# Optimization experiments

Hardware: AMD Instinct MI355X
Metric: run time of the kernel (lower is better)

Reference implementation:

```python
import jax, jax.numpy as jnp
import numpy as np

N = 50000    # nodes
P = 4        # meta-paths
E = 800000   # edges per meta-path (avg degree 16)
IN = 256     # in_size
OUT = 128    # out_size


def _xavier(key, shape, gain=1.0):
    fan_in, fan_out = shape[-2], shape[-1]
    lim = gain * np.sqrt(6.0 / (fan_in + fan_out))
    return jax.random.uniform(key, shape, jnp.float32, -lim, lim)


def setup_inputs() -> dict:
    key = jax.random.key(0)
    ks = jax.random.split(key, 8)
    x = jax.random.normal(ks[0], (N, IN), jnp.float32)
    src = jax.random.randint(ks[1], (P, E), 0, N)
    dst = jax.random.randint(ks[2], (P, E), 0, N)
    # per-meta-path GraphConv weight/bias (dgl default: xavier weight, zero bias)
    W = _xavier(ks[3], (P, IN, OUT))
    b_conv = jnp.zeros((P, OUT), jnp.float32)
    # semantic attention vectors, xavier with gain=1.414 on shape (1, OUT)
    att_lim = 1.414 * np.sqrt(6.0 / (1 + OUT))
    att = jax.random.uniform(ks[4], (P, OUT), jnp.float32, -att_lim, att_lim)
    fc_w = _xavier(ks[5], (OUT, OUT))
    fc_b = jnp.zeros((OUT,), jnp.float32)
    h_bias = jnp.zeros((OUT,), jnp.float32)
    return {"x": x, "W": W, "b_conv": b_conv, "att": att,
            "fc_w": fc_w, "fc_b": fc_b, "h_bias": h_bias,
            "src": src, "dst": dst}


def _graphconv(x, src, dst, W, b):
    # dgl GraphConv, norm='both', allow_zero_in_degree=True (degrees clamped to 1)
    ones_e = jnp.ones(src.shape[0], x.dtype)
    deg_out = jnp.maximum(jax.ops.segment_sum(ones_e, src, num_segments=N), 1.0)
    deg_in = jnp.maximum(jax.ops.segment_sum(ones_e, dst, num_segments=N), 1.0)
    # weight applied before aggregation (in_size > out_size path) -- same math
    xw = (x * jax.lax.rsqrt(deg_out)[:, None]) @ W          # [N, OUT]
    agg = jax.ops.segment_sum(xw[src], dst, num_segments=N)  # [N, OUT]
    return agg * jax.lax.rsqrt(deg_in)[:, None] + b


def reference(x, W, b_conv, att, fc_w, fc_b, h_bias, src, dst):
    # one GraphConv per meta-path (P is a small fixed structural set)
    hs = [_graphconv(x, src[i], dst[i], W[i], b_conv[i]) for i in range(P)]
    # semantic attention: sp_i = tanh(fc(h_i)).mean(0); beta_i = att_i . sp_i
    sp = jnp.stack([jnp.tanh(h @ fc_w.T + fc_b).mean(axis=0) for h in hs])  # [P, OUT]
    beta = jax.nn.softmax(jnp.sum(att * sp, axis=-1))  # [P]
    h = hs[0] * beta[0]
    for i in range(1, P):
        h = h + hs[i] * beta[i]
    # epilogue: bias (self_loop=False, activation=None, dropout eval = identity)
    return h + h_bias
```

## Files before the change

### kernel.cpp

```cpp
#include <hip/hip_runtime.h>
#include <math.h>

#define N_NODES 50000
#define P_PATHS 4
#define E_EDGES 800000
#define IN_F 256
#define OUT_F 128
#define NPB 128
#define NBUCK 391
#define NCHUNK 200
#define CHUNK_E (E_EDGES / NCHUNK)
#define GBLK 391
#define DSL 20
#define QTR 4
#define Q_N 12500
#define Q_W 6250
#define AP 264
#define FP 136
#define RSB 196

typedef unsigned short ushort_t;
typedef unsigned int uint_t;
typedef float f32x4 __attribute__((ext_vector_type(4)));
typedef short s16x8 __attribute__((ext_vector_type(8)));

__device__ __forceinline__ ushort_t f2bf(float f) {
    uint_t u = __float_as_uint(f);
    return (ushort_t)((u + 0x7FFFu + ((u >> 16) & 1u)) >> 16);
}
__device__ __forceinline__ float bf2f(ushort_t h) {
    return __uint_as_float(((uint_t)h) << 16);
}

__global__ void prep_kernel(const float* __restrict__ W, const float* __restrict__ fcw,
                            ushort_t* __restrict__ Wt, ushort_t* __restrict__ fcwb)
{
    int idx = blockIdx.x * blockDim.x + threadIdx.x;
    if (idx < P_PATHS * IN_F * OUT_F) {
        int p = idx >> 15;
        int r = idx & 32767;
        int k = r >> 7;
        int n = r & 127;
        Wt[((size_t)p << 15) + (size_t)n * IN_F + k] = f2bf(W[idx]);
    }
    if (idx < OUT_F * OUT_F) fcwb[idx] = f2bf(fcw[idx]);
}

__global__ __launch_bounds__(256) void deghist_kernel(const int* __restrict__ src,
                                                      const int* __restrict__ dst,
                                                      uint_t* __restrict__ dhist,
                                                      uint_t* __restrict__ bcounts)
{
    __shared__ uint_t cnt[Q_W];
    int sl = blockIdx.x, q = blockIdx.y, p = blockIdx.z;
    int t = threadIdx.x;
    if (q == QTR) {
        for (int i = t; i < NBUCK; i += 256) cnt[i] = 0;
        __syncthreads();
        const int4* d4 = (const int4*)(dst + (size_t)p * E_EDGES + (size_t)sl * (E_EDGES / DSL));
        for (int i = t; i < E_EDGES / DSL / 4; i += 256) {
            int4 v = d4[i];
            atomicAdd(&cnt[v.x >> 7], 1u);
            atomicAdd(&cnt[v.y >> 7], 1u);
            atomicAdd(&cnt[v.z >> 7], 1u);
            atomicAdd(&cnt[v.w >> 7], 1u);
        }
        __syncthreads();
        for (int i = t; i < NBUCK; i += 256)
            if (cnt[i]) atomicAdd(&bcounts[p * NBUCK + i], cnt[i]);
        return;
    }
    int nbase = q * Q_N;
    for (int i = t; i < Q_W; i += 256) cnt[i] = 0;
    __syncthreads();
    const int4* s4 = (const int4*)(src + (size_t)p * E_EDGES + (size_t)sl * (E_EDGES / DSL));
    for (int i = t; i < E_EDGES / DSL / 4; i += 256) {
        int4 v = s4[i];
        uint_t r;
        r = (uint_t)(v.x - nbase); if (r < Q_N) atomicAdd(&cnt[r >> 1], 1u << ((r & 1) * 16));
        r = (uint_t)(v.y - nbase); if (r < Q_N) atomicAdd(&cnt[r >> 1], 1u << ((r & 1) * 16));
        r = (uint_t)(v.z - nbase); if (r < Q_N) atomicAdd(&cnt[r >> 1], 1u << ((r & 1) * 16));
        r = (uint_t)(v.w - nbase); if (r < Q_N) atomicAdd(&cnt[r >> 1], 1u << ((r & 1) * 16));
    }
    __syncthreads();
    uint_t* outp = dhist + (((size_t)p * QTR + q) * DSL + sl) * Q_W;
    for (int i = t; i < Q_W; i += 256) outp[i] = cnt[i];
}

__global__ __launch_bounds__(1024) void rsout_bscan_kernel(const uint_t* __restrict__ dhist,
                                                           float* __restrict__ rsout,
                                                           const uint_t* __restrict__ bcounts,
                                                           int* __restrict__ bstart,
                                                           int* __restrict__ bcursor)
{
    int t = threadIdx.x;
    if (blockIdx.x == RSB) {
        __shared__ int a[2048], b[2048];
        for (int i = t; i < 2048; i += 1024)
            a[i] = (i < P_PATHS * NBUCK) ? (int)bcounts[i] : 0;
        __syncthreads();
        int* pin = a; int* pout = b;
        for (int off = 1; off < 2048; off <<= 1) {
            for (int i = t; i < 2048; i += 1024)
                pout[i] = pin[i] + (i >= off ? pin[i - off] : 0);
            __syncthreads();
            int* tmp = pin; pin = pout; pout = tmp;
        }
        for (int i = t; i < P_PATHS * NBUCK; i += 1024) {
            int st = pin[i] - (int)bcounts[i];
            bstart[i] = st;
            bcursor[i] = st;
        }
        if (t == 0) bstart[P_PATHS * NBUCK] = pin[P_PATHS * NBUCK - 1];
        return;
    }
    int idx = blockIdx.x * 1024 + t;
    if (idx >= P_PATHS * QTR * Q_W) return;
    int ph = idx / Q_W;
    int w  = idx % Q_W;
    const uint_t* base = dhist + (size_t)ph * DSL * Q_W + w;
    uint_t s = 0;
#pragma unroll
    for (int sl = 0; sl < DSL; ++sl) s += base[(size_t)sl * Q_W];
    int p = ph >> 2, q = ph & 3;
    int node = q * Q_N + 2 * w;
    uint_t c0 = s & 0xFFFFu, c1 = s >> 16;
    rsout[(size_t)p * N_NODES + node]     = rsqrtf((float)(c0 ? c0 : 1u));
    rsout[(size_t)p * N_NODES + node + 1] = rsqrtf((float)(c1 ? c1 : 1u));
}

__global__ __launch_bounds__(256) void bscatter_kernel(const int* __restrict__ src,
                                                       const int* __restrict__ dst,
                                                       int* __restrict__ bcursor,
                                                       uint_t* __restrict__ ebuf)
{
    __shared__ uint_t bh[NBUCK];
    __shared__ uint_t lbase[NBUCK];
    int p = blockIdx.y;
    int t = threadIdx.x;
    int sub = p * E_EDGES;
    int* bcursor_p = bcursor + p * NBUCK;
    uint_t* ebuf_p = ebuf + (size_t)p * E_EDGES;
    for (int i = t; i < NBUCK; i += 256) bh[i] = 0;
    __syncthreads();
    size_t ebase = (size_t)p * E_EDGES + (size_t)blockIdx.x * CHUNK_E;
    const int4* d4 = (const int4*)(dst + ebase);
    const int4* s4 = (const int4*)(src + ebase);
    for (int i = t; i < CHUNK_E / 4; i += 256) {
        int4 v = d4[i];
        atomicAdd(&bh[v.x >> 7], 1u);
        atomicAdd(&bh[v.y >> 7], 1u);
        atomicAdd(&bh[v.z >> 7], 1u);
        atomicAdd(&bh[v.w >> 7], 1u);
    }
    __syncthreads();
    for (int i = t; i < NBUCK; i += 256) {
        uint_t c = bh[i];
        lbase[i] = c ? (uint_t)(atomicAdd(&bcursor_p[i], (int)c) - sub) : 0u;
        bh[i] = 0;
    }
    __syncthreads();
    for (int i = t; i < CHUNK_E / 4; i += 256) {
        int4 d = d4[i];
        int4 s = s4[i];
        { int bk = d.x >> 7; uint_t pos = lbase[bk] + atomicAdd(&bh[bk], 1u); ebuf_p[pos] = (uint_t)s.x | ((uint_t)(d.x & 127) << 16); }
        { int bk = d.y >> 7; uint_t pos = lbase[bk] + atomicAdd(&bh[bk], 1u); ebuf_p[pos] = (uint_t)s.y | ((uint_t)(d.y & 127) << 16); }
        { int bk = d.z >> 7; uint_t pos = lbase[bk] + atomicAdd(&bh[bk], 1u); ebuf_p[pos] = (uint_t)s.z | ((uint_t)(d.z & 127) << 16); }
        { int bk = d.w >> 7; uint_t pos = lbase[bk] + atomicAdd(&bh[bk], 1u); ebuf_p[pos] = (uint_t)s.w | ((uint_t)(d.w & 127) << 16); }
    }
}

__global__ __launch_bounds__(256) void blocal_kernel(const uint_t* __restrict__ ebuf,
                                                     const int* __restrict__ bstart,
                                                     ushort_t* __restrict__ eidx2,
                                                     int* __restrict__ rsn)
{
    __shared__ uint_t hist[NPB];
    __shared__ uint_t cur[NPB];
    __shared__ uint_t sa[NPB], sb[NPB];
    int bkt = blockIdx.x;
    int p = blockIdx.y;
    int t = threadIdx.x;
    int sub = p * E_EDGES;
    const uint_t* ebuf_p = ebuf + (size_t)p * E_EDGES;
    ushort_t* eidx2_p = eidx2 + (size_t)p * E_EDGES;
    int* rsn_p = rsn + (size_t)p * (N_NODES + 1);
    if (t < NPB) hist[t] = 0;
    __syncthreads();
    int r0 = bstart[p * NBUCK + bkt] - sub;
    int r1 = bstart[p * NBUCK + bkt + 1] - sub;
    for (int e = r0 + t; e < r1; e += 256)
        atomicAdd(&hist[ebuf_p[e] >> 16], 1u);
    __syncthreads();
    if (t < NPB) sa[t] = hist[t];
    __syncthreads();
    uint_t* pin = sa; uint_t* pout = sb;
    for (int off = 1; off < NPB; off <<= 1) {
        if (t < NPB) pout[t] = pin[t] + (t >= off ? pin[t - off] : 0u);
        __syncthreads();
        uint_t* tmp = pin; pin = pout; pout = tmp;
    }
    if (t < NPB) {
        uint_t ex = pin[t] - hist[t];
        int node = bkt * NPB + t;
        if (node < N_NODES) rsn_p[node] = r0 + (int)ex;
        cur[t] = ex;
    }
    if (bkt == NBUCK - 1 && t == 0) rsn_p[N_NODES] = r1;
    __syncthreads();
    for (int e = r0 + t; e < r1; e += 256) {
        uint_t pk = ebuf_p[e];
        int dl = (int)(pk >> 16);
        uint_t pos = atomicAdd(&cur[dl], 1u);
        eidx2_p[r0 + pos] = (ushort_t)(pk & 0xFFFFu);
    }
}

__global__ __launch_bounds__(256) void gemm_xall_kernel(const float* __restrict__ x,
                                                        const ushort_t* __restrict__ Wt,
                                                        const float* __restrict__ rsout,
                                                        ushort_t* __restrict__ xwb)
{
    __shared__ ushort_t As[128 * AP];
    __shared__ ushort_t Bs[128 * AP];
    int m0 = blockIdx.x * 128;
    int t = threadIdx.x;
    int wid = t >> 6, lane = t & 63;
    int wr = wid >> 1, wc = wid & 1;
    int srow = t >> 1, half = (t & 1) * 16;
    int gr = m0 + srow;
#pragma unroll
    for (int c = 0; c < 8; ++c) {
        int kb = c * 32 + half;
        uint4 w0 = make_uint4(0, 0, 0, 0), w1 = make_uint4(0, 0, 0, 0);
        if (gr < N_NODES) {
            const float* ap = x + (size_t)gr * IN_F + kb;
            float4 f0 = *(const float4*)(ap + 0);
            float4 f1 = *(const float4*)(ap + 4);
            float4 f2 = *(const float4*)(ap + 8);
            float4 f3 = *(const float4*)(ap + 12);
            w0.x = (uint_t)f2bf(f0.x) | ((uint_t)f2bf(f0.y) << 16);
            w0.y = (uint_t)f2bf(f0.z) | ((uint_t)f2bf(f0.w) << 16);
            w0.z = (uint_t)f2bf(f1.x) | ((uint_t)f2bf(f1.y) << 16);
            w0.w = (uint_t)f2bf(f1.z) | ((uint_t)f2bf(f1.w) << 16);
            w1.x = (uint_t)f2bf(f2.x) | ((uint_t)f2bf(f2.y) << 16);
            w1.y = (uint_t)f2bf(f2.z) | ((uint_t)f2bf(f2.w) << 16);
            w1.z = (uint_t)f2bf(f3.x) | ((uint_t)f2bf(f3.y) << 16);
            w1.w = (uint_t)f2bf(f3.z) | ((uint_t)f2bf(f3.w) << 16);
        }
        *(uint4*)&As[srow * AP + kb]     = w0;
        *(uint4*)&As[srow * AP + kb + 8] = w1;
    }
    for (int pp = 0; pp < 2; ++pp) {
        int p = blockIdx.y * 2 + pp;
        __syncthreads();
        const ushort_t* Wp = Wt + ((size_t)p << 15);
#pragma unroll
        for (int c = 0; c < 8; ++c) {
            int kb = c * 32 + half;
            const ushort_t* bp = Wp + (size_t)srow * IN_F + kb;
            *(uint4*)&Bs[srow * AP + kb]     = *(const uint4*)(bp);
            *(uint4*)&Bs[srow * AP + kb + 8] = *(const uint4*)(bp + 8);
        }
        __syncthreads();
        f32x4 acc[4][4] = {};
#pragma unroll
        for (int k0 = 0; k0 < IN_F; k0 += 32) {
            s16x8 aF[4], bF[4];
            int kk = k0 + (lane >> 4) * 8;
#pragma unroll
            for (int m = 0; m < 4; ++m)
                aF[m] = *(const s16x8*)&As[(wr * 64 + m * 16 + (lane & 15)) * AP + kk];
#pragma unroll
            for (int n = 0; n < 4; ++n)
                bF[n] = *(const s16x8*)&Bs[(wc * 64 + n * 16 + (lane & 15)) * AP + kk];
#pragma unroll
            for (int m = 0; m < 4; ++m)
#pragma unroll
                for (int n = 0; n < 4; ++n)
                    acc[m][n] = __builtin_amdgcn_mfma_f32_16x16x32_bf16(aF[m], bF[n], acc[m][n], 0, 0, 0);
        }
        ushort_t* xp = xwb + (size_t)p * N_NODES * OUT_F;
        const float* rp = rsout + (size_t)p * N_NODES;
#pragma unroll
        for (int m = 0; m < 4; ++m) {
#pragma unroll
            for (int i = 0; i < 4; ++i) {
                int row = m0 + wr * 64 + m * 16 + (lane >> 4) * 4 + i;
                if (row < N_NODES) {
                    float rs = rp[row];
#pragma unroll
                    for (int n = 0; n < 4; ++n) {
                        int col = wc * 64 + n * 16 + (lane & 15);
                        xp[(size_t)row * OUT_F + col] = f2bf(acc[m][n][i] * rs);
                    }
                }
            }
        }
    }
}

__global__ __launch_bounds__(256) void gather_kernel(const ushort_t* __restrict__ xwb,
                                                     const ushort_t* __restrict__ eidx2,
                                                     const int* __restrict__ rsn,
                                                     const float* __restrict__ bconv,
                                                     uint_t* __restrict__ hb)
{
    int wid = threadIdx.x >> 6, lane = threadIdx.x & 63;
    int p = blockIdx.y;
    int n0 = (blockIdx.x * 4 + wid) * 2;
    const int* rsn_p = rsn + (size_t)p * (N_NODES + 1);
    const ushort_t* eidx2_p = eidx2 + (size_t)p * E_EDGES;
    int bA = rsn_p[n0], mid = rsn_p[n0 + 1], eB = rsn_p[n0 + 2];
    const uint_t* base = (const uint_t*)xwb + (size_t)p * N_NODES * 64 + lane;
    float a0 = 0.f, a1 = 0.f, b0 = 0.f, b1 = 0.f;
    int iA = bA, iB = mid;
    while (iA + 4 <= mid && iB + 4 <= eB) {
        int sA0 = eidx2_p[iA], sA1 = eidx2_p[iA + 1], sA2 = eidx2_p[iA + 2], sA3 = eidx2_p[iA + 3];
        int sB0 = eidx2_p[iB], sB1 = eidx2_p[iB + 1], sB2 = eidx2_p[iB + 2], sB3 = eidx2_p[iB + 3];
        uint_t wA0 = base[(size_t)sA0 * 64];
        uint_t wA1 = base[(size_t)sA1 * 64];
        uint_t wA2 = base[(size_t)sA2 * 64];
        uint_t wA3 = base[(size_t)sA3 * 64];
        uint_t wB0 = base[(size_t)sB0 * 64];
        uint_t wB1 = base[(size_t)sB1 * 64];
        uint_t wB2 = base[(size_t)sB2 * 64];
        uint_t wB3 = base[(size_t)sB3 * 64];
        a0 += (bf2f((ushort_t)wA0) + bf2f((ushort_t)wA1)) + (bf2f((ushort_t)wA2) + bf2f((ushort_t)wA3));
        a1 += (bf2f((ushort_t)(wA0 >> 16)) + bf2f((ushort_t)(wA1 >> 16))) +
              (bf2f((ushort_t)(wA2 >> 16)) + bf2f((ushort_t)(wA3 >> 16)));
        b0 += (bf2f((ushort_t)wB0) + bf2f((ushort_t)wB1)) + (bf2f((ushort_t)wB2) + bf2f((ushort_t)wB3));
        b1 += (bf2f((ushort_t)(wB0 >> 16)) + bf2f((ushort_t)(wB1 >> 16))) +
              (bf2f((ushort_t)(wB2 >> 16)) + bf2f((ushort_t)(wB3 >> 16)));
        iA += 4; iB += 4;
    }
    for (; iA + 4 <= mid; iA += 4) {
        int s0 = eidx2_p[iA], s1 = eidx2_p[iA + 1], s2 = eidx2_p[iA + 2], s3 = eidx2_p[iA + 3];
        uint_t w0 = base[(size_t)s0 * 64];
        uint_t w1 = base[(size_t)s1 * 64];
        uint_t w2 = base[(size_t)s2 * 64];
        uint_t w3 = base[(size_t)s3 * 64];
        a0 += (bf2f((ushort_t)w0) + bf2f((ushort_t)w1)) + (bf2f((ushort_t)w2) + bf2f((ushort_t)w3));
        a1 += (bf2f((ushort_t)(w0 >> 16)) + bf2f((ushort_t)(w1 >> 16))) +
              (bf2f((ushort_t)(w2 >> 16)) + bf2f((ushort_t)(w3 >> 16)));
    }
    for (; iA < mid; ++iA) {
        uint_t w = base[(size_t)eidx2_p[iA] * 64];
        a0 += bf2f((ushort_t)w);
        a1 += bf2f((ushort_t)(w >> 16));
    }
    for (; iB + 4 <= eB; iB += 4) {
        int s0 = eidx2_p[iB], s1 = eidx2_p[iB + 1], s2 = eidx2_p[iB + 2], s3 = eidx2_p[iB + 3];
        uint_t w0 = base[(size_t)s0 * 64];
        uint_t w1 = base[(size_t)s1 * 64];
        uint_t w2 = base[(size_t)s2 * 64];
        uint_t w3 = base[(size_t)s3 * 64];
        b0 += (bf2f((ushort_t)w0) + bf2f((ushort_t)w1)) + (bf2f((ushort_t)w2) + bf2f((ushort_t)w3));
        b1 += (bf2f((ushort_t)(w0 >> 16)) + bf2f((ushort_t)(w1 >> 16))) +
              (bf2f((ushort_t)(w2 >> 16)) + bf2f((ushort_t)(w3 >> 16)));
    }
    for (; iB < eB; ++iB) {
        uint_t w = base[(size_t)eidx2_p[iB] * 64];
        b0 += bf2f((ushort_t)w);
        b1 += bf2f((ushort_t)(w >> 16));
    }
    int dA = mid - bA, dB = eB - mid;
    float scA = rsqrtf((float)(dA > 0 ? dA : 1));
    float scB = rsqrtf((float)(dB > 0 ? dB : 1));
    float2 bc = *(const float2*)(bconv + (size_t)p * OUT_F + 2 * lane);
    hb[((size_t)p * N_NODES + n0) * 64 + lane] =
        (uint_t)f2bf(fmaf(a0, scA, bc.x)) | ((uint_t)f2bf(fmaf(a1, scA, bc.y)) << 16);
    hb[((size_t)p * N_NODES + n0 + 1) * 64 + lane] =
        (uint_t)f2bf(fmaf(b0, scB, bc.x)) | ((uint_t)f2bf(fmaf(b1, scB, bc.y)) << 16);
}

__global__ __launch_bounds__(256) void fc_mfma_kernel(const ushort_t* __restrict__ hb,
                                                      const ushort_t* __restrict__ fcwb,
                                                      const float* __restrict__ fcb,
                                                      float* __restrict__ partial)
{
    __shared__ ushort_t As[128 * FP];
    __shared__ ushort_t Bs[128 * FP];
    __shared__ float red[2][128];
    int m0 = blockIdx.x * 128;
    int p = blockIdx.y;
    int t = threadIdx.x;
    int wid = t >> 6, lane = t & 63;
    int wr = wid >> 1, wc = wid & 1;
    int srow = t >> 1, half = (t & 1) * 16;
    int gr = m0 + srow;
    const ushort_t* hp = hb + (size_t)p * N_NODES * OUT_F;
#pragma unroll
    for (int c = 0; c < 4; ++c) {
        int kb = c * 32 + half;
        uint4 w0 = make_uint4(0, 0, 0, 0), w1 = make_uint4(0, 0, 0, 0);
        if (gr < N_NODES) {
            const ushort_t* ap = hp + (size_t)gr * OUT_F + kb;
            w0 = *(const uint4*)(ap);
            w1 = *(const uint4*)(ap + 8);
        }
        *(uint4*)&As[srow * FP + kb]     = w0;
        *(uint4*)&As[srow * FP + kb + 8] = w1;
        const ushort_t* bp = fcwb + (size_t)srow * OUT_F + kb;
        *(uint4*)&Bs[srow * FP + kb]     = *(const uint4*)(bp);
        *(uint4*)&Bs[srow * FP + kb + 8] = *(const uint4*)(bp + 8);
    }
    __syncthreads();
    f32x4 acc[4][4] = {};
#pragma unroll
    for (int k0 = 0; k0 < OUT_F; k0 += 32) {
        s16x8 aF[4], bF[4];
        int kk = k0 + (lane >> 4) * 8;
#pragma unroll
        for (int m = 0; m < 4; ++m)
            aF[m] = *(const s16x8*)&As[(wr * 64 + m * 16 + (lane & 15)) * FP + kk];
#pragma unroll
        for (int n = 0; n < 4; ++n)
            bF[n] = *(const s16x8*)&Bs[(wc * 64 + n * 16 + (lane & 15)) * FP + kk];
#pragma unroll
        for (int m = 0; m < 4; ++m)
#pragma unroll
            for (int n = 0; n < 4; ++n)
                acc[m][n] = __builtin_amdgcn_mfma_f32_16x16x32_bf16(aF[m], bF[n], acc[m][n], 0, 0, 0);
    }
#pragma unroll
    for (int n = 0; n < 4; ++n) {
        int col = wc * 64 + n * 16 + (lane & 15);
        float fb = fcb[col];
        float s = 0.f;
#pragma unroll
        for (int m = 0; m < 4; ++m)
#pragma unroll
            for (int i = 0; i < 4; ++i) {
                int row = m0 + wr * 64 + m * 16 + (lane >> 4) * 4 + i;
                if (row < N_NODES) s += tanhf(acc[m][n][i] + fb);
            }
        s += __shfl_xor(s, 16);
        s += __shfl_xor(s, 32);
        if (lane < 16) red[wr][col] = s;
    }
    __syncthreads();
    if (t < 128)
        partial[((size_t)p * GBLK + blockIdx.x) * OUT_F + t] = red[0][t] + red[1][t];
}

__global__ __launch_bounds__(512) void beta_reduce_kernel(const float* __restrict__ partial,
                                                          const float* __restrict__ att,
                                                          float* __restrict__ beta)
{
    int t = threadIdx.x;
    int p = t >> 7, c = t & 127;
    float s = 0.f;
    for (int i = 0; i < GBLK; ++i)
        s += partial[((size_t)p * GBLK + i) * OUT_F + c];
    float v = att[p * OUT_F + c] * (s * (1.0f / N_NODES));
    __shared__ float red[512];
    red[t] = v;
    __syncthreads();
    for (int off = 64; off >= 1; off >>= 1) {
        if (c < off) red[t] += red[t + off];
        __syncthreads();
    }
    if (t == 0) {
        float w[P_PATHS], mx = -1e30f;
        for (int q = 0; q < P_PATHS; ++q) { w[q] = red[q * 128]; mx = fmaxf(mx, w[q]); }
        float sum = 0.f;
        for (int q = 0; q < P_PATHS; ++q) { w[q] = expf(w[q] - mx); sum += w[q]; }
        for (int q = 0; q < P_PATHS; ++q) beta[q] = w[q] / sum;
    }
}

__global__ void combine_kernel(const uint_t* __restrict__ hb, const float* __restrict__ hbias,
                               const float* __restrict__ beta, float* __restrict__ out)
{
    int idx = blockIdx.x * blockDim.x + threadIdx.x;
    if (idx >= N_NODES * 64) return;
    int n = idx >> 6;
    int w = idx & 63;
    float2 hbv = *(const float2*)(hbias + 2 * w);
    float r0 = hbv.x, r1 = hbv.y;
#pragma unroll
    for (int p = 0; p < P_PATHS; ++p) {
        float bp = beta[p];
        uint_t v = hb[((size_t)p * N_NODES + n) * 64 + w];
        r0 = fmaf(bp, bf2f((ushort_t)v), r0);
        r1 = fmaf(bp, bf2f((ushort_t)(v >> 16)), r1);
    }
    *(float2*)(out + (size_t)n * OUT_F + 2 * w) = make_float2(r0, r1);
}

extern "C" void kernel_launch(void* const* d_in, const int* in_sizes, int n_in,
                              void* d_out, int out_size, void* d_ws, size_t ws_size,
                              hipStream_t stream)
{
    const float* x      = (const float*)d_in[0];
    const float* W      = (const float*)d_in[1];
    const float* b_conv = (const float*)d_in[2];
    const float* att    = (const float*)d_in[3];
    const float* fc_w   = (const float*)d_in[4];
    const float* fc_b   = (const float*)d_in[5];
    const float* h_bias = (const float*)d_in[6];
    const int*   src    = (const int*)d_in[7];
    const int*   dst    = (const int*)d_in[8];
    float* out = (float*)d_out;
    float* ws  = (float*)d_ws;

    size_t off_rsout   = 0;
    size_t off_partial = off_rsout + (size_t)P_PATHS * N_NODES;
    size_t off_beta    = off_partial + (size_t)P_PATHS * GBLK * OUT_F;
    size_t off_i32     = (off_beta + 4 + 63) & ~(size_t)63;
    size_t i_bstart  = 0;
    size_t i_bcursor = 1600;
    size_t i_bcounts = 3200;
    size_t i_rsn     = 4800;
    size_t i_dhist   = 204864;
    size_t i_ebuf    = i_dhist + (size_t)P_PATHS * QTR * DSL * Q_W;
    size_t n_ints    = i_ebuf + (size_t)P_PATHS * E_EDGES;
    size_t off_u16   = off_i32 + ((n_ints + 63) & ~(size_t)63);
    size_t u_hb    = 0;
    size_t u_xwb   = u_hb + (size_t)P_PATHS * N_NODES * OUT_F;
    size_t u_eidx2 = u_xwb + (size_t)P_PATHS * N_NODES * OUT_F;
    size_t u_Wt    = u_eidx2 + (size_t)P_PATHS * E_EDGES;
    size_t u_fcwb  = u_Wt + (size_t)P_PATHS * IN_F * OUT_F;

    float* rsout   = ws + off_rsout;
    float* partial = ws + off_partial;
    float* beta    = ws + off_beta;
    int*   ibase   = (int*)(ws + off_i32);
    int*    bstart  = ibase + i_bstart;
    int*    bcursor = ibase + i_bcursor;
    uint_t* bcounts = (uint_t*)(ibase + i_bcounts);
    int*    rsn     = ibase + i_rsn;
    uint_t* dhist   = (uint_t*)(ibase + i_dhist);
    uint_t* ebuf    = (uint_t*)(ibase + i_ebuf);
    ushort_t* ubase = (ushort_t*)(ws + off_u16);
    ushort_t* hb    = ubase + u_hb;
    ushort_t* xwb   = ubase + u_xwb;
    ushort_t* eidx2 = ubase + u_eidx2;
    ushort_t* Wt    = ubase + u_Wt;
    ushort_t* fcwb  = ubase + u_fcwb;

    hipMemsetAsync(bcounts, 0, (size_t)P_PATHS * NBUCK * sizeof(uint_t), stream);

    prep_kernel<<<(P_PATHS * IN_F * OUT_F + 255) / 256, 256, 0, stream>>>(W, fc_w, Wt, fcwb);
    deghist_kernel<<<dim3(DSL, QTR + 1, P_PATHS), 256, 0, stream>>>(src, dst, dhist, bcounts);
    rsout_bscan_kernel<<<RSB + 1, 1024, 0, stream>>>(dhist, rsout, bcounts, bstart, bcursor);

    gemm_xall_kernel<<<dim3(GBLK, 2), 256, 0, stream>>>(x, Wt, rsout, xwb);
    bscatter_kernel<<<dim3(NCHUNK, P_PATHS), 256, 0, stream>>>(src, dst, bcursor, ebuf);
    blocal_kernel<<<dim3(NBUCK, P_PATHS), 256, 0, stream>>>(ebuf, bstart, eidx2, rsn);
    gather_kernel<<<dim3(N_NODES / 8, P_PATHS), 256, 0, stream>>>(
        xwb, eidx2, rsn, b_conv, (uint_t*)hb);
    fc_mfma_kernel<<<dim3(GBLK, P_PATHS), 256, 0, stream>>>(hb, fcwb, fc_b, partial);

    beta_reduce_kernel<<<1, 512, 0, stream>>>(partial, att, beta);
    combine_kernel<<<(N_NODES * 64 + 255) / 256, 256, 0, stream>>>(
        (const uint_t*)hb, h_bias, beta, out);
}
```

Before: 331.2 us.

## Tile GEMM over K, widen gather loads, loop paths in fc kernel, fast tanh

The x@W GEMM now streams K in 64-wide tiles instead of staging the full 256-wide A and B tiles in LDS. This shrinks shared memory use per block and may allow more blocks per CU, but it re-reads and re-converts x for each of the two paths. The gather kernel uses 32-lane half-waves that each load 8 bytes per edge, so more nodes are handled per block. The fc kernel loads fc_w once and loops over the four paths, and it replaces tanhf with an exp-based approximation.

```diff
diff --git a/kernel.cpp b/kernel.cpp
--- a/kernel.cpp
+++ b/kernel.cpp
@@ -15,7 +15,7 @@
 #define QTR 4
 #define Q_N 12500
 #define Q_W 6250
-#define AP 264
+#define BKP 72
 #define FP 136
 #define RSB 196
 
@@ -30,6 +30,25 @@
 }
 __device__ __forceinline__ float bf2f(ushort_t h) {
     return __uint_as_float(((uint_t)h) << 16);
+}
+__device__ __forceinline__ uint4 pack8(const float4 f0, const float4 f1) {
+    uint4 w;
+    w.x = (uint_t)f2bf(f0.x) | ((uint_t)f2bf(f0.y) << 16);
+    w.y = (uint_t)f2bf(f0.z) | ((uint_t)f2bf(f0.w) << 16);
+    w.z = (uint_t)f2bf(f1.x) | ((uint_t)f2bf(f1.y) << 16);
+    w.w = (uint_t)f2bf(f1.z) | ((uint_t)f2bf(f1.w) << 16);
+    return w;
+}
+__device__ __forceinline__ float fast_tanh(float v) {
+    v = fminf(fmaxf(v, -20.f), 20.f);
+    float ex = __expf(2.f * v);
+    return (ex - 1.f) / (ex + 1.f);
+}
+__device__ __forceinline__ void acc4(float4& a, uint2 w) {
+    a.x += bf2f((ushort_t)w.x);
+    a.y += bf2f((ushort_t)(w.x >> 16));
+    a.z += bf2f((ushort_t)w.y);
+    a.w += bf2f((ushort_t)(w.y >> 16));
 }
 
 __global__ void prep_kernel(const float* __restrict__ W, const float* __restrict__ fcw,
@@ -221,64 +240,55 @@
                                                         const float* __restrict__ rsout,
                                                         ushort_t* __restrict__ xwb)
 {
-    __shared__ ushort_t As[128 * AP];
-    __shared__ ushort_t Bs[128 * AP];
+    __shared__ ushort_t As[128 * BKP];
+    __shared__ ushort_t Bs[128 * BKP];
     int m0 = blockIdx.x * 128;
     int t = threadIdx.x;
     int wid = t >> 6, lane = t & 63;
     int wr = wid >> 1, wc = wid & 1;
-    int srow = t >> 1, half = (t & 1) * 16;
+    int srow = t >> 1, h32 = (t & 1) * 32;
     int gr = m0 + srow;
-#pragma unroll
-    for (int c = 0; c < 8; ++c) {
-        int kb = c * 32 + half;
-        uint4 w0 = make_uint4(0, 0, 0, 0), w1 = make_uint4(0, 0, 0, 0);
-        if (gr < N_NODES) {
-            const float* ap = x + (size_t)gr * IN_F + kb;
-            float4 f0 = *(const float4*)(ap + 0);
-            float4 f1 = *(const float4*)(ap + 4);
-            float4 f2 = *(const float4*)(ap + 8);
-            float4 f3 = *(const float4*)(ap + 12);
-            w0.x = (uint_t)f2bf(f0.x) | ((uint_t)f2bf(f0.y) << 16);
-            w0.y = (uint_t)f2bf(f0.z) | ((uint_t)f2bf(f0.w) << 16);
-            w0.z = (uint_t)f2bf(f1.x) | ((uint_t)f2bf(f1.y) << 16);
-            w0.w = (uint_t)f2bf(f1.z) | ((uint_t)f2bf(f1.w) << 16);
-            w1.x = (uint_t)f2bf(f2.x) | ((uint_t)f2bf(f2.y) << 16);
-            w1.y = (uint_t)f2bf(f2.z) | ((uint_t)f2bf(f2.w) << 16);
-            w1.z = (uint_t)f2bf(f3.x) | ((uint_t)f2bf(f3.y) << 16);
-            w1.w = (uint_t)f2bf(f3.z) | ((uint_t)f2bf(f3.w) << 16);
-        }
-        *(uint4*)&As[srow * AP + kb]     = w0;
-        *(uint4*)&As[srow * AP + kb + 8] = w1;
-    }
     for (int pp = 0; pp < 2; ++pp) {
         int p = blockIdx.y * 2 + pp;
-        __syncthreads();
         const ushort_t* Wp = Wt + ((size_t)p << 15);
-#pragma unroll
-        for (int c = 0; c < 8; ++c) {
-            int kb = c * 32 + half;
-            const ushort_t* bp = Wp + (size_t)srow * IN_F + kb;
-            *(uint4*)&Bs[srow * AP + kb]     = *(const uint4*)(bp);
-            *(uint4*)&Bs[srow * AP + kb + 8] = *(const uint4*)(bp + 8);
-        }
-        __syncthreads();
         f32x4 acc[4][4] = {};
-#pragma unroll
-        for (int k0 = 0; k0 < IN_F; k0 += 32) {
-            s16x8 aF[4], bF[4];
-            int kk = k0 + (lane >> 4) * 8;
-#pragma unroll
-            for (int m = 0; m < 4; ++m)
-                aF[m] = *(const s16x8*)&As[(wr * 64 + m * 16 + (lane & 15)) * AP + kk];
-#pragma unroll
-            for (int n = 0; n < 4; ++n)
-                bF[n] = *(const s16x8*)&Bs[(wc * 64 + n * 16 + (lane & 15)) * AP + kk];
-#pragma unroll
-            for (int m = 0; m < 4; ++m)
+        for (int kt = 0; kt < 4; ++kt) {
+            __syncthreads();
+            {
+                const float* ap = x + (size_t)gr * IN_F + kt * 64 + h32;
+#pragma unroll
+                for (int c = 0; c < 4; ++c) {
+                    float4 f0 = make_float4(0.f, 0.f, 0.f, 0.f), f1 = f0;
+                    if (gr < N_NODES) {
+                        f0 = *(const float4*)(ap + c * 8);
+                        f1 = *(const float4*)(ap + c * 8 + 4);
+                    }
+                    *(uint4*)&As[srow * BKP + h32 + c * 8] = pack8(f0, f1);
+                }
+            }
+            {
+                const ushort_t* bp = Wp + (size_t)srow * IN_F + kt * 64 + h32;
+#pragma unroll
+                for (int c = 0; c < 4; ++c)
+                    *(uint4*)&Bs[srow * BKP + h32 + c * 8] = *(const uint4*)(bp + c * 8);
+            }
+            __syncthreads();
+#pragma unroll
+            for (int k0 = 0; k0 < 64; k0 += 32) {
+                s16x8 aF[4], bF[4];
+                int kk = k0 + (lane >> 4) * 8;
+#pragma unroll
+                for (int m = 0; m < 4; ++m)
+                    aF[m] = *(const s16x8*)&As[(wr * 64 + m * 16 + (lane & 15)) * BKP + kk];
 #pragma unroll
                 for (int n = 0; n < 4; ++n)
-                    acc[m][n] = __builtin_amdgcn_mfma_f32_16x16x32_bf16(aF[m], bF[n], acc[m][n], 0, 0, 0);
+                    bF[n] = *(const s16x8*)&Bs[(wc * 64 + n * 16 + (lane & 15)) * BKP + kk];
+#pragma unroll
+                for (int m = 0; m < 4; ++m)
+#pragma unroll
+                    for (int n = 0; n < 4; ++n)
+                        acc[m][n] = __builtin_amdgcn_mfma_f32_16x16x32_bf16(aF[m], bF[n], acc[m][n], 0, 0, 0);
+            }
         }
         ushort_t* xp = xwb + (size_t)p * N_NODES * OUT_F;
         const float* rp = rsout + (size_t)p * N_NODES;
@@ -304,74 +314,69 @@
                                                      const ushort_t* __restrict__ eidx2,
                                                      const int* __restrict__ rsn,
                                                      const float* __restrict__ bconv,
-                                                     uint_t* __restrict__ hb)
-{
-    int wid = threadIdx.x >> 6, lane = threadIdx.x & 63;
+                                                     uint2* __restrict__ hb)
+{
+    int hw = threadIdx.x >> 5;
+    int lane = threadIdx.x & 31;
     int p = blockIdx.y;
-    int n0 = (blockIdx.x * 4 + wid) * 2;
+    int n0 = (blockIdx.x * 8 + hw) * 2;
     const int* rsn_p = rsn + (size_t)p * (N_NODES + 1);
     const ushort_t* eidx2_p = eidx2 + (size_t)p * E_EDGES;
     int bA = rsn_p[n0], mid = rsn_p[n0 + 1], eB = rsn_p[n0 + 2];
-    const uint_t* base = (const uint_t*)xwb + (size_t)p * N_NODES * 64 + lane;
-    float a0 = 0.f, a1 = 0.f, b0 = 0.f, b1 = 0.f;
+    const uint2* base = (const uint2*)xwb + (size_t)p * N_NODES * 32 + lane;
+    float4 aA = make_float4(0.f, 0.f, 0.f, 0.f);
+    float4 aB = make_float4(0.f, 0.f, 0.f, 0.f);
     int iA = bA, iB = mid;
     while (iA + 4 <= mid && iB + 4 <= eB) {
         int sA0 = eidx2_p[iA], sA1 = eidx2_p[iA + 1], sA2 = eidx2_p[iA + 2], sA3 = eidx2_p[iA + 3];
         int sB0 = eidx2_p[iB], sB1 = eidx2_p[iB + 1], sB2 = eidx2_p[iB + 2], sB3 = eidx2_p[iB + 3];
-        uint_t wA0 = base[(size_t)sA0 * 64];
-        uint_t wA1 = base[(size_t)sA1 * 64];
-        uint_t wA2 = base[(size_t)sA2 * 64];
-        uint_t wA3 = base[(size_t)sA3 * 64];
-        uint_t wB0 = base[(size_t)sB0 * 64];
-        uint_t wB1 = base[(size_t)sB1 * 64];
-        uint_t wB2 = base[(size_t)sB2 * 64];
-        uint_t wB3 = base[(size_t)sB3 * 64];
-        a0 += (bf2f((ushort_t)wA0) + bf2f((ushort_t)wA1)) + (bf2f((ushort_t)wA2) + bf2f((ushort_t)wA3));
-        a1 += (bf2f((ushort_t)(wA0 >> 16)) + bf2f((ushort_t)(wA1 >> 16))) +
-              (bf2f((ushort_t)(wA2 >> 16)) + bf2f((ushort_t)(wA3 >> 16)));
-        b0 += (bf2f((ushort_t)wB0) + bf2f((ushort_t)wB1)) + (bf2f((ushort_t)wB2) + bf2f((ushort_t)wB3));
-        b1 += (bf2f((ushort_t)(wB0 >> 16)) + bf2f((ushort_t)(wB1 >> 16))) +
-              (bf2f((ushort_t)(wB2 >> 16)) + bf2f((ushort_t)(wB3 >> 16)));
+        uint2 wA0 = base[(size_t)sA0 * 32];
+        uint2 wA1 = base[(size_t)sA1 * 32];
+        uint2 wA2 = base[(size_t)sA2 * 32];
+        uint2 wA3 = base[(size_t)sA3 * 32];
+        uint2 wB0 = base[(size_t)sB0 * 32];
+        uint2 wB1 = base[(size_t)sB1 * 32];
+        uint2 wB2 = base[(size_t)sB2 * 32];
+        uint2 wB3 = base[(size_t)sB3 * 32];
+        acc4(aA, wA0); acc4(aA, wA1); acc4(aA, wA2); acc4(aA, wA3);
+        acc4(aB, wB0); acc4(aB, wB1); acc4(aB, wB2); acc4(aB, wB3);
         iA += 4; iB += 4;
     }
     for (; iA + 4 <= mid; iA += 4) {
         int s0 = eidx2_p[iA], s1 = eidx2_p[iA + 1], s2 = eidx2_p[iA + 2], s3 = eidx2_p[iA + 3];
-        uint_t w0 = base[(size_t)s0 * 64];
-        uint_t w1 = base[(size_t)s1 * 64];
-        uint_t w2 = base[(size_t)s2 * 64];
-        uint_t w3 = base[(size_t)s3 * 64];
-        a0 += (bf2f((ushort_t)w0) + bf2f((ushort_t)w1)) + (bf2f((ushort_t)w2) + bf2f((ushort_t)w3));
-        a1 += (bf2f((ushort_t)(w0 >> 16)) + bf2f((ushort_t)(w1 >> 16))) +
-              (bf2f((ushort_t)(w2 >> 16)) + bf2f((ushort_t)(w3 >> 16)));
+        uint2 w0 = base[(size_t)s0 * 32];
+        uint2 w1 = base[(size_t)s1 * 32];
+        uint2 w2 = base[(size_t)s2 * 32];
+        uint2 w3 = base[(size_t)s3 * 32];
+        acc4(aA, w0); acc4(aA, w1); acc4(aA, w2); acc4(aA, w3);
     }
     for (; iA < mid; ++iA) {
-        uint_t w = base[(size_t)eidx2_p[iA] * 64];
-        a0 += bf2f((ushort_t)w);
-        a1 += bf2f((ushort_t)(w >> 16));
+        uint2 w = base[(size_t)eidx2_p[iA] * 32];
+        acc4(aA, w);
     }
     for (; iB + 4 <= eB; iB += 4) {
         int s0 = eidx2_p[iB], s1 = eidx2_p[iB + 1], s2 = eidx2_p[iB + 2], s3 = eidx2_p[iB + 3];
-        uint_t w0 = base[(size_t)s0 * 64];
-        uint_t w1 = base[(size_t)s1 * 64];
-        uint_t w2 = base[(size_t)s2 * 64];
-        uint_t w3 = base[(size_t)s3 * 64];
-        b0 += (bf2f((ushort_t)w0) + bf2f((ushort_t)w1)) + (bf2f((ushort_t)w2) + bf2f((ushort_t)w3));
-        b1 += (bf2f((ushort_t)(w0 >> 16)) + bf2f((ushort_t)(w1 >> 16))) +
-              (bf2f((ushort_t)(w2 >> 16)) + bf2f((ushort_t)(w3 >> 16)));
+        uint2 w0 = base[(size_t)s0 * 32];
+        uint2 w1 = base[(size_t)s1 * 32];
+        uint2 w2 = base[(size_t)s2 * 32];
+        uint2 w3 = base[(size_t)s3 * 32];
+        acc4(aB, w0); acc4(aB, w1); acc4(aB, w2); acc4(aB, w3);
     }
     for (; iB < eB; ++iB) {
-        uint_t w = base[(size_t)eidx2_p[iB] * 64];
-        b0 += bf2f((ushort_t)w);
-        b1 += bf2f((ushort_t)(w >> 16));
+        uint2 w = base[(size_t)eidx2_p[iB] * 32];
+        acc4(aB, w);
     }
     int dA = mid - bA, dB = eB - mid;
     float scA = rsqrtf((float)(dA > 0 ? dA : 1));
     float scB = rsqrtf((float)(dB > 0 ? dB : 1));
-    float2 bc = *(const float2*)(bconv + (size_t)p * OUT_F + 2 * lane);
-    hb[((size_t)p * N_NODES + n0) * 64 + lane] =
-        (uint_t)f2bf(fmaf(a0, scA, bc.x)) | ((uint_t)f2bf(fmaf(a1, scA, bc.y)) << 16);
-    hb[((size_t)p * N_NODES + n0 + 1) * 64 + lane] =
-        (uint_t)f2bf(fmaf(b0, scB, bc.x)) | ((uint_t)f2bf(fmaf(b1, scB, bc.y)) << 16);
+    float4 bc = *(const float4*)(bconv + (size_t)p * OUT_F + lane * 4);
+    uint2 oA, oB;
+    oA.x = (uint_t)f2bf(fmaf(aA.x, scA, bc.x)) | ((uint_t)f2bf(fmaf(aA.y, scA, bc.y)) << 16);
+    oA.y = (uint_t)f2bf(fmaf(aA.z, scA, bc.z)) | ((uint_t)f2bf(fmaf(aA.w, scA, bc.w)) << 16);
+    oB.x = (uint_t)f2bf(fmaf(aB.x, scB, bc.x)) | ((uint_t)f2bf(fmaf(aB.y, scB, bc.y)) << 16);
+    oB.y = (uint_t)f2bf(fmaf(aB.z, scB, bc.z)) | ((uint_t)f2bf(fmaf(aB.w, scB, bc.w)) << 16);
+    hb[((size_t)p * N_NODES + n0) * 32 + lane]     = oA;
+    hb[((size_t)p * N_NODES + n0 + 1) * 32 + lane] = oB;
 }
 
 __global__ __launch_bounds__(256) void fc_mfma_kernel(const ushort_t* __restrict__ hb,
@@ -383,65 +388,73 @@
     __shared__ ushort_t Bs[128 * FP];
     __shared__ float red[2][128];
     int m0 = blockIdx.x * 128;
-    int p = blockIdx.y;
     int t = threadIdx.x;
     int wid = t >> 6, lane = t & 63;
     int wr = wid >> 1, wc = wid & 1;
     int srow = t >> 1, half = (t & 1) * 16;
     int gr = m0 + srow;
-    const ushort_t* hp = hb + (size_t)p * N_NODES * OUT_F;
-#pragma unroll
-    for (int c = 0; c < 4; ++c) {
-        int kb = c * 32 + half;
-        uint4 w0 = make_uint4(0, 0, 0, 0), w1 = make_uint4(0, 0, 0, 0);
-        if (gr < N_NODES) {
-            const ushort_t* ap = hp + (size_t)gr * OUT_F + kb;
-            w0 = *(const uint4*)(ap);
-            w1 = *(const uint4*)(ap + 8);
-        }
-        *(uint4*)&As[srow * FP + kb]     = w0;
-        *(uint4*)&As[srow * FP + kb + 8] = w1;
-        const ushort_t* bp = fcwb + (size_t)srow * OUT_F + kb;
-        *(uint4*)&Bs[srow * FP + kb]     = *(const uint4*)(bp);
-        *(uint4*)&Bs[srow * FP + kb + 8] = *(const uint4*)(bp + 8);
-    }
-    __syncthreads();
-    f32x4 acc[4][4] = {};
-#pragma unroll
-    for (int k0 = 0; k0 < OUT_F; k0 += 32) {
-        s16x8 aF[4], bF[4];
-        int kk = k0 + (lane >> 4) * 8;
-#pragma unroll
-        for (int m = 0; m < 4; ++m)
-            aF[m] = *(const s16x8*)&As[(wr * 64 + m * 16 + (lane & 15)) * FP + kk];
-#pragma unroll
-        for (int n = 0; n < 4; ++n)
-            bF[n] = *(const s16x8*)&Bs[(wc * 64 + n * 16 + (lane & 15)) * FP + kk];
-#pragma unroll
-        for (int m = 0; m < 4; ++m)
+    {
+#pragma unroll
+        for (int c = 0; c < 4; ++c) {
+            int kb = c * 32 + half;
+            const ushort_t* bp = fcwb + (size_t)srow * OUT_F + kb;
+            *(uint4*)&Bs[srow * FP + kb]     = *(const uint4*)(bp);
+            *(uint4*)&Bs[srow * FP + kb + 8] = *(const uint4*)(bp + 8);
+        }
+    }
+    for (int p = 0; p < P_PATHS; ++p) {
+        __syncthreads();
+        const ushort_t* hp = hb + (size_t)p * N_NODES * OUT_F;
+#pragma unroll
+        for (int c = 0; c < 4; ++c) {
+            int kb = c * 32 + half;
+            uint4 w0 = make_uint4(0, 0, 0, 0), w1 = w0;
+            if (gr < N_NODES) {
+                const ushort_t* ap = hp + (size_t)gr * OUT_F + kb;
+                w0 = *(const uint4*)(ap);
+                w1 = *(const uint4*)(ap + 8);
+            }
+            *(uint4*)&As[srow * FP + kb]     = w0;
+            *(uint4*)&As[srow * FP + kb + 8] = w1;
+        }
+        __syncthreads();
+        f32x4 acc[4][4] = {};
+#pragma unroll
+        for (int k0 = 0; k0 < OUT_F; k0 += 32) {
+            s16x8 aF[4], bF[4];
+            int kk = k0 + (lane >> 4) * 8;
+#pragma unroll
+            for (int m = 0; m < 4; ++m)
+                aF[m] = *(const s16x8*)&As[(wr * 64 + m * 16 + (lane & 15)) * FP + kk];
 #pragma unroll
             for (int n = 0; n < 4; ++n)
-                acc[m][n] = __builtin_amdgcn_mfma_f32_16x16x32_bf16(aF[m], bF[n], acc[m][n], 0, 0, 0);
-    }
-#pragma unroll
-    for (int n = 0; n < 4; ++n) {
-        int col = wc * 64 + n * 16 + (lane & 15);
-        float fb = fcb[col];
-        float s = 0.f;
-#pragma unroll
-        for (int m = 0; m < 4; ++m)
-#pragma unroll
-            for (int i = 0; i < 4; ++i) {
-                int row = m0 + wr * 64 + m * 16 + (lane >> 4) * 4 + i;
-                if (row < N_NODES) s += tanhf(acc[m][n][i] + fb);
-            }
-        s += __shfl_xor(s, 16);
-        s += __shfl_xor(s, 32);
-        if (lane < 16) red[wr][col] = s;
-    }
-    __syncthreads();
-    if (t < 128)
-        partial[((size_t)p * GBLK + blockIdx.x) * OUT_F + t] = red[0][t] + red[1][t];
+                bF[n] = *(const s16x8*)&Bs[(wc * 64 + n * 16 + (lane & 15)) * FP + kk];
+#pragma unroll
+            for (int m = 0; m < 4; ++m)
+#pragma unroll
+                for (int n = 0; n < 4; ++n)
+                    acc[m][n] = __builtin_amdgcn_mfma_f32_16x16x32_bf16(aF[m], bF[n], acc[m][n], 0, 0, 0);
+        }
+#pragma unroll
+        for (int n = 0; n < 4; ++n) {
+            int col = wc * 64 + n * 16 + (lane & 15);
+            float fb = fcb[col];
+            float s = 0.f;
+#pragma unroll
+            for (int m = 0; m < 4; ++m)
+#pragma unroll
+                for (int i = 0; i < 4; ++i) {
+                    int row = m0 + wr * 64 + m * 16 + (lane >> 4) * 4 + i;
+                    if (row < N_NODES) s += fast_tanh(acc[m][n][i] + fb);
+                }
+            s += __shfl_xor(s, 16);
+            s += __shfl_xor(s, 32);
+            if (lane < 16) red[wr][col] = s;
+        }
+        __syncthreads();
+        if (t < 128)
+            partial[((size_t)p * GBLK + blockIdx.x) * OUT_F + t] = red[0][t] + red[1][t];
+    }
 }
 
 __global__ __launch_bounds__(512) void beta_reduce_kernel(const float* __restrict__ partial,
@@ -549,9 +562,9 @@
     gemm_xall_kernel<<<dim3(GBLK, 2), 256, 0, stream>>>(x, Wt, rsout, xwb);
     bscatter_kernel<<<dim3(NCHUNK, P_PATHS), 256, 0, stream>>>(src, dst, bcursor, ebuf);
     blocal_kernel<<<dim3(NBUCK, P_PATHS), 256, 0, stream>>>(ebuf, bstart, eidx2, rsn);
-    gather_kernel<<<dim3(N_NODES / 8, P_PATHS), 256, 0, stream>>>(
-        xwb, eidx2, rsn, b_conv, (uint_t*)hb);
-    fc_mfma_kernel<<<dim3(GBLK, P_PATHS), 256, 0, stream>>>(hb, fcwb, fc_b, partial);
+    gather_kernel<<<dim3(N_NODES / 16, P_PATHS), 256, 0, stream>>>(
+        xwb, eidx2, rsn, b_conv, (uint2*)hb);
+    fc_mfma_kernel<<<GBLK, 256, 0, stream>>>(hb, fcwb, fc_b, partial);
 
     beta_reduce_kernel<<<1, 512, 0, stream>>>(partial, att, beta);
     combine_kernel<<<(N_NODES * 64 + 255) / 256, 256, 0, stream>>>(
```

Measured after the change: 316.6 us. 1.05x faster.
